# Performance work log

Hardware: AMD Instinct MI355X
Metric: run time of the kernel (lower is better)

## Reference

```python
import jax, jax.numpy as jnp
import numpy as np

T, B, DIN, DLAT = 512, 64, 256, 512

def setup_inputs() -> dict:
    key = jax.random.key(0)
    ks = jax.random.split(key, 5)
    return {
        "x": jax.random.normal(ks[0], (T, B, DIN), dtype=jnp.float32),
        "h0": jax.random.normal(ks[1], (B, DLAT), dtype=jnp.float32),
        "W_in": jax.random.normal(ks[2], (DLAT, DIN), dtype=jnp.float32) * (1.0 / np.sqrt(DIN)),
        "W_h": jax.random.normal(ks[3], (DLAT, DLAT), dtype=jnp.float32) * (1.0 / np.sqrt(DLAT)),
        "b_h": jax.random.normal(ks[4], (DLAT,), dtype=jnp.float32) * 0.01,
    }

def reference(x, h0, W_in, W_h, b_h):
    # x: [T, B, dim_in]; h0: [B, dim_latent]
    # one_step: relu(x @ W_in^T + h @ W_h^T + b_h); stack hidden states over time
    def step(h, x_t):
        h_new = jax.nn.relu(x_t @ W_in.T + h @ W_h.T + b_h)
        return h_new, h_new
    _, h_seq = jax.lax.scan(step, h0, x)  # h_seq: [T, B, dim_latent]
    return h_seq
```

## Files before the change

kernel.cpp:

```cpp
#include <hip/hip_runtime.h>

#define TSTEPS 512
#define BATCH  64
#define DIN    256
#define DLAT   512

typedef _Float16 half8_t __attribute__((ext_vector_type(8)));
typedef float    f32x4  __attribute__((ext_vector_type(4)));

#define WS_WF_OFF  (512u * 1024u)
#define WS_TIER2   (512u * 1024u)
#define WS_TIER1   (768u * 1024u)

__device__ __forceinline__ void barrier_lds_only()
{
    __builtin_amdgcn_sched_barrier(0);
    asm volatile("s_waitcnt lgkmcnt(0)\n\ts_barrier" ::: "memory");
    __builtin_amdgcn_sched_barrier(0);
}

#define BM 64
#define BN 64
#define BK 32

__global__ __launch_bounds__(256)
void precompute_gemm(const float* __restrict__ x,
                     const float* __restrict__ Win,
                     const float* __restrict__ bh,
                     float* __restrict__ P)
{
    __shared__ float As[BM][BK + 1];
    __shared__ float Ws[BN][BK + 1];
    const int m0  = blockIdx.y * BM;
    const int n0  = blockIdx.x * BN;
    const int tid = threadIdx.x;
    const int tx  = tid & 15;
    const int ty  = tid >> 4;
    const int lr  = tid >> 2;
    const int lc  = (tid & 3) * 8;

    float acc[4][4] = {};

    for (int kk = 0; kk < DIN; kk += BK) {
        const float* ax = x   + (size_t)(m0 + lr) * DIN + kk + lc;
        const float* aw = Win + (size_t)(n0 + lr) * DIN + kk + lc;
        float4 a0 = *(const float4*)(ax);
        float4 a1 = *(const float4*)(ax + 4);
        float4 w0 = *(const float4*)(aw);
        float4 w1 = *(const float4*)(aw + 4);
        As[lr][lc+0]=a0.x; As[lr][lc+1]=a0.y; As[lr][lc+2]=a0.z; As[lr][lc+3]=a0.w;
        As[lr][lc+4]=a1.x; As[lr][lc+5]=a1.y; As[lr][lc+6]=a1.z; As[lr][lc+7]=a1.w;
        Ws[lr][lc+0]=w0.x; Ws[lr][lc+1]=w0.y; Ws[lr][lc+2]=w0.z; Ws[lr][lc+3]=w0.w;
        Ws[lr][lc+4]=w1.x; Ws[lr][lc+5]=w1.y; Ws[lr][lc+6]=w1.z; Ws[lr][lc+7]=w1.w;
        __syncthreads();
        #pragma unroll
        for (int k = 0; k < BK; ++k) {
            float a[4], w[4];
            #pragma unroll
            for (int i = 0; i < 4; ++i) a[i] = As[ty*4+i][k];
            #pragma unroll
            for (int j = 0; j < 4; ++j) w[j] = Ws[tx*4+j][k];
            #pragma unroll
            for (int i = 0; i < 4; ++i)
                #pragma unroll
                for (int j = 0; j < 4; ++j)
                    acc[i][j] += a[i] * w[j];
        }
        __syncthreads();
    }

    float4 bv = *(const float4*)(bh + n0 + tx*4);
    #pragma unroll
    for (int i = 0; i < 4; ++i) {
        float4 v;
        v.x = acc[i][0] + bv.x; v.y = acc[i][1] + bv.y;
        v.z = acc[i][2] + bv.z; v.w = acc[i][3] + bv.w;
        *(float4*)(P + (size_t)(m0 + ty*4 + i) * DLAT + n0 + tx*4) = v;
    }
}

__global__ __launch_bounds__(256)
void pack_wh_mfma(const float* __restrict__ Wh, _Float16* __restrict__ Wm)
{
    const int idx  = blockIdx.x * 256 + threadIdx.x;
    const int lane = idx & 63;
    const int tile = idx >> 6;
    const int kt   = tile >> 5;
    const int ntg  = tile & 31;
    const int n    = ntg * 16 + (lane & 15);
    const int k0   = kt * 32 + (lane >> 4) * 8;
    half8_t v;
    #pragma unroll
    for (int e = 0; e < 8; ++e)
        v[e] = (_Float16)Wh[(size_t)n * DLAT + k0 + e];
    *(half8_t*)(Wm + (size_t)idx * 8) = v;
}

__global__ __launch_bounds__(256)
void pack_win_f16(const float* __restrict__ Win, _Float16* __restrict__ Wf)
{
    const int idx  = blockIdx.x * 256 + threadIdx.x;
    const int lane = idx & 63;
    const int tile = idx >> 6;
    const int kt   = tile >> 5;
    const int ntg  = tile & 31;
    const int n    = ntg * 16 + (lane & 15);
    const int k0   = kt * 32 + (lane >> 4) * 8;
    half8_t v;
    #pragma unroll
    for (int e = 0; e < 8; ++e)
        v[e] = (_Float16)Win[(size_t)n * DIN + k0 + e];
    *(half8_t*)(Wf + (size_t)idx * 8) = v;
}

__global__ __launch_bounds__(256)
void precompute_mfma(const float* __restrict__ x,
                     const half8_t* __restrict__ Wf,
                     const float* __restrict__ bh,
                     float* __restrict__ P)
{
    const int tid  = threadIdx.x;
    const int wave = tid >> 6, lane = tid & 63;
    const int wm   = wave >> 1, wn = wave & 1;
    const int m0   = (blockIdx.x >> 2) * 128 + wm * 64;
    const int n0   = (blockIdx.x & 3) * 128 + wn * 64;
    const int col  = lane & 15, rg = lane >> 4;

    float bv[4];
    #pragma unroll
    for (int nt = 0; nt < 4; ++nt) bv[nt] = bh[n0 + nt * 16 + col];

    f32x4 C[4][4] = {};

    #pragma unroll
    for (int kt = 0; kt < 8; ++kt) {
        half8_t A[4];
        #pragma unroll
        for (int mt = 0; mt < 4; ++mt) {
            const float* xp = x + (size_t)(m0 + mt * 16 + col) * DIN
                                + kt * 32 + rg * 8;
            float4 a = *(const float4*)xp;
            float4 b = *(const float4*)(xp + 4);
            half8_t v;
            v[0] = (_Float16)a.x; v[1] = (_Float16)a.y;
            v[2] = (_Float16)a.z; v[3] = (_Float16)a.w;
            v[4] = (_Float16)b.x; v[5] = (_Float16)b.y;
            v[6] = (_Float16)b.z; v[7] = (_Float16)b.w;
            A[mt] = v;
        }
        half8_t B[4];
        #pragma unroll
        for (int nt = 0; nt < 4; ++nt)
            B[nt] = Wf[(size_t)((kt * 32 + (n0 >> 4) + nt) * 64) + lane];
        #pragma unroll
        for (int mt = 0; mt < 4; ++mt)
            #pragma unroll
            for (int nt = 0; nt < 4; ++nt)
                C[mt][nt] = __builtin_amdgcn_mfma_f32_16x16x32_f16(
                                A[mt], B[nt], C[mt][nt], 0, 0, 0);
    }

    #pragma unroll
    for (int mt = 0; mt < 4; ++mt)
        #pragma unroll
        for (int nt = 0; nt < 4; ++nt) {
            #pragma unroll
            for (int r = 0; r < 4; ++r) {
                const int m = m0 + mt * 16 + rg * 4 + r;
                P[(size_t)m * DLAT + n0 + nt * 16 + col] = C[mt][nt][r] + bv[nt];
            }
        }
}

__global__ __launch_bounds__(512, 2)
void rnn_scan_pf(const half8_t* __restrict__ Wm,
                 const float* __restrict__ h0,
                 float* __restrict__ out)
{
    __shared__ half8_t  ldsB[8 * 16 * 64];
    __shared__ _Float16 hbuf[2][DLAT];

    const int b    = blockIdx.x;
    const int tid  = threadIdx.x;
    const int w    = tid >> 6;
    const int lane = tid & 63;
    const int kt0  = 2 * w;
    const int aoff = (lane >> 4) * 8;

    half8_t bfr[48];
    #pragma unroll
    for (int s = 0; s < 16; ++s) {
        const int c  = s >> 1;
        const int kt = (kt0 + s) & 15;
        #pragma unroll
        for (int nt = 0; nt < 4; ++nt) {
            half8_t v = Wm[(size_t)((kt * 32 + w * 4 + nt) * 64) + lane];
            if ((s & 1) && nt >= 2) ldsB[(w * 16 + c * 2 + (nt - 2)) * 64 + lane] = v;
            else                    bfr[c * 6 + ((s & 1) ? 4 + nt : nt)] = v;
        }
    }

    hbuf[0][tid] = (_Float16)h0[(size_t)b * DLAT + tid];
    __syncthreads();

    half8_t Ap[2][2], Bp[2];
    #pragma unroll
    for (int i = 0; i < 4; ++i)
        Ap[i >> 1][i & 1] =
            *(const half8_t*)&hbuf[0][((kt0 + i) & 15) * 32 + aoff];
    Bp[0] = ldsB[(w * 16 + 0) * 64 + lane];
    Bp[1] = ldsB[(w * 16 + 1) * 64 + lane];

    for (int t = 0; t < TSTEPS; ++t) {
        const int cur = t & 1, nxt = cur ^ 1;
        float* orow = out + ((size_t)t * BATCH + b) * DLAT;
        float pv = orow[w * 64 + lane];

        f32x4 C[4] = {};
        __builtin_amdgcn_s_setprio(1);
        #pragma unroll
        for (int c = 0; c < 8; ++c) {
            const int pb = c & 1;
            #pragma unroll
            for (int nt = 0; nt < 4; ++nt)
                C[nt] = __builtin_amdgcn_mfma_f32_16x16x32_f16(
                            Ap[pb][0], bfr[c * 6 + nt], C[nt], 0, 0, 0);
            C[0] = __builtin_amdgcn_mfma_f32_16x16x32_f16(
                        Ap[pb][1], bfr[c * 6 + 4], C[0], 0, 0, 0);
            C[1] = __builtin_amdgcn_mfma_f32_16x16x32_f16(
                        Ap[pb][1], bfr[c * 6 + 5], C[1], 0, 0, 0);
            C[2] = __builtin_amdgcn_mfma_f32_16x16x32_f16(
                        Ap[pb][1], Bp[0], C[2], 0, 0, 0);
            C[3] = __builtin_amdgcn_mfma_f32_16x16x32_f16(
                        Ap[pb][1], Bp[1], C[3], 0, 0, 0);
            if (c < 7) {
                Bp[0] = ldsB[(w * 16 + (c + 1) * 2 + 0) * 64 + lane];
                Bp[1] = ldsB[(w * 16 + (c + 1) * 2 + 1) * 64 + lane];
            }
            if (c < 6) {
                #pragma unroll
                for (int i = 0; i < 2; ++i) {
                    const int s = (c + 2) * 2 + i;
                    Ap[pb][i] =
                        *(const half8_t*)&hbuf[cur][((kt0 + s) & 15) * 32 + aoff];
                }
            }
        }
        __builtin_amdgcn_s_setprio(0);

        const int g4 = lane >> 4;
        float m = (g4 == 0) ? C[0][0]
                : (g4 == 1) ? C[1][0]
                : (g4 == 2) ? C[2][0]
                :             C[3][0];
        float v = fmaxf(m + pv, 0.f);
        orow[w * 64 + lane] = v;
        hbuf[nxt][w * 64 + lane] = (_Float16)v;

        Ap[0][0] = *(const half8_t*)&hbuf[nxt][((kt0 + 0) & 15) * 32 + aoff];
        Ap[0][1] = *(const half8_t*)&hbuf[nxt][((kt0 + 1) & 15) * 32 + aoff];
        Bp[0] = ldsB[(w * 16 + 0) * 64 + lane];
        Bp[1] = ldsB[(w * 16 + 1) * 64 + lane];

        barrier_lds_only();

        Ap[1][0] = *(const half8_t*)&hbuf[nxt][((kt0 + 2) & 15) * 32 + aoff];
        Ap[1][1] = *(const half8_t*)&hbuf[nxt][((kt0 + 3) & 15) * 32 + aoff];
    }
}

__global__ __launch_bounds__(512)
void rnn_scan_row(const float* __restrict__ Wh,
                  const float* __restrict__ h0,
                  float* __restrict__ out)
{
    __shared__ float h[DLAT];
    const int b = blockIdx.x;
    const int r = threadIdx.x;
    h[r] = h0[(size_t)b * DLAT + r];
    __syncthreads();
    const float* wrow = Wh + (size_t)r * DLAT;
    for (int t = 0; t < TSTEPS; ++t) {
        float* orow = out + ((size_t)t * BATCH + b) * DLAT;
        float acc = orow[r];
        #pragma unroll 8
        for (int k = 0; k < DLAT; k += 4) {
            float4 w  = *(const float4*)(wrow + k);
            float4 hv = *(const float4*)&h[k];
            acc += w.x*hv.x + w.y*hv.y + w.z*hv.z + w.w*hv.w;
        }
        float v = fmaxf(acc, 0.f);
        __syncthreads();
        h[r] = v;
        orow[r] = v;
        __syncthreads();
    }
}

extern "C" void kernel_launch(void* const* d_in, const int* in_sizes, int n_in,
                              void* d_out, int out_size, void* d_ws, size_t ws_size,
                              hipStream_t stream)
{
    const float* x    = (const float*)d_in[0];
    const float* h0   = (const float*)d_in[1];
    const float* Win  = (const float*)d_in[2];
    const float* Wh   = (const float*)d_in[3];
    const float* bh   = (const float*)d_in[4];
    float* out = (float*)d_out;

    if (ws_size >= WS_TIER1) {
        _Float16* Wm = (_Float16*)d_ws;
        _Float16* Wf = (_Float16*)((char*)d_ws + WS_WF_OFF);
        pack_wh_mfma<<<128, 256, 0, stream>>>(Wh, Wm);
        pack_win_f16<<<64, 256, 0, stream>>>(Win, Wf);
        precompute_mfma<<<1024, 256, 0, stream>>>(x, (const half8_t*)Wf, bh, out);
        rnn_scan_pf<<<BATCH, 512, 0, stream>>>((const half8_t*)Wm, h0, out);
    } else if (ws_size >= WS_TIER2) {
        _Float16* Wm = (_Float16*)d_ws;
        dim3 gA(DLAT / BN, (TSTEPS * BATCH) / BM);
        pack_wh_mfma<<<128, 256, 0, stream>>>(Wh, Wm);
        precompute_gemm<<<gA, 256, 0, stream>>>(x, Win, bh, out);
        rnn_scan_pf<<<BATCH, 512, 0, stream>>>((const half8_t*)Wm, h0, out);
    } else {
        dim3 gA(DLAT / BN, (TSTEPS * BATCH) / BM);
        precompute_gemm<<<gA, 256, 0, stream>>>(x, Win, bh, out);
        rnn_scan_row<<<BATCH, 512, 0, stream>>>(Wh, h0, out);
    }
}
```

Measured before the change: 676.2 us.

## Run own-wave MFMA chunk before barrier and prefetch next-step input projection

Each wave's first K-chunk reads only the hidden-state slice that the same wave just wrote. The recurrent scan now issues those eight MFMAs before the per-step LDS barrier instead of after it. This takes part of the matrix work off the serial barrier-to-barrier critical path of every timestep. The precomputed input projection for the next timestep is also loaded from global memory one step early, so its latency is hidden behind the current step. The cost is more live registers and a peeled prologue, and correctness depends on the chunk-0 k-tiles staying within the wave's own output slice.

```diff
diff --git a/kernel.cpp b/kernel.cpp
--- a/kernel.cpp
+++ b/kernel.cpp
@@ -173,7 +173,7 @@
 }
 
 __global__ __launch_bounds__(512, 2)
-void rnn_scan_pf(const half8_t* __restrict__ Wm,
+void rnn_scan_pb(const half8_t* __restrict__ Wm,
                  const float* __restrict__ h0,
                  float* __restrict__ out)
 {
@@ -203,23 +203,39 @@
     hbuf[0][tid] = (_Float16)h0[(size_t)b * DLAT + tid];
     __syncthreads();
 
+#define CHUNK0_EXEC()                                                          \
+    do {                                                                       \
+        C[0] = __builtin_amdgcn_mfma_f32_16x16x32_f16(Ap[0][0], bfr[0], C[0], 0, 0, 0); \
+        C[1] = __builtin_amdgcn_mfma_f32_16x16x32_f16(Ap[0][0], bfr[1], C[1], 0, 0, 0); \
+        C[2] = __builtin_amdgcn_mfma_f32_16x16x32_f16(Ap[0][0], bfr[2], C[2], 0, 0, 0); \
+        C[3] = __builtin_amdgcn_mfma_f32_16x16x32_f16(Ap[0][0], bfr[3], C[3], 0, 0, 0); \
+        C[0] = __builtin_amdgcn_mfma_f32_16x16x32_f16(Ap[0][1], bfr[4], C[0], 0, 0, 0); \
+        C[1] = __builtin_amdgcn_mfma_f32_16x16x32_f16(Ap[0][1], bfr[5], C[1], 0, 0, 0); \
+        C[2] = __builtin_amdgcn_mfma_f32_16x16x32_f16(Ap[0][1], Bp[0],  C[2], 0, 0, 0); \
+        C[3] = __builtin_amdgcn_mfma_f32_16x16x32_f16(Ap[0][1], Bp[1],  C[3], 0, 0, 0); \
+    } while (0)
+
     half8_t Ap[2][2], Bp[2];
-    #pragma unroll
-    for (int i = 0; i < 4; ++i)
-        Ap[i >> 1][i & 1] =
-            *(const half8_t*)&hbuf[0][((kt0 + i) & 15) * 32 + aoff];
+    f32x4 C[4] = {};
+    Ap[0][0] = *(const half8_t*)&hbuf[0][((kt0 + 0) & 15) * 32 + aoff];
+    Ap[0][1] = *(const half8_t*)&hbuf[0][((kt0 + 1) & 15) * 32 + aoff];
     Bp[0] = ldsB[(w * 16 + 0) * 64 + lane];
     Bp[1] = ldsB[(w * 16 + 1) * 64 + lane];
+    CHUNK0_EXEC();
+    Bp[0] = ldsB[(w * 16 + 2) * 64 + lane];
+    Bp[1] = ldsB[(w * 16 + 3) * 64 + lane];
+    Ap[1][0] = *(const half8_t*)&hbuf[0][((kt0 + 2) & 15) * 32 + aoff];
+    Ap[1][1] = *(const half8_t*)&hbuf[0][((kt0 + 3) & 15) * 32 + aoff];
+    Ap[0][0] = *(const half8_t*)&hbuf[0][((kt0 + 4) & 15) * 32 + aoff];
+    Ap[0][1] = *(const half8_t*)&hbuf[0][((kt0 + 5) & 15) * 32 + aoff];
+    float pvt = out[(size_t)0 * BATCH * DLAT + (size_t)b * DLAT + w * 64 + lane];
 
     for (int t = 0; t < TSTEPS; ++t) {
         const int cur = t & 1, nxt = cur ^ 1;
-        float* orow = out + ((size_t)t * BATCH + b) * DLAT;
-        float pv = orow[w * 64 + lane];
-
-        f32x4 C[4] = {};
+
         __builtin_amdgcn_s_setprio(1);
         #pragma unroll
-        for (int c = 0; c < 8; ++c) {
+        for (int c = 1; c < 8; ++c) {
             const int pb = c & 1;
             #pragma unroll
             for (int nt = 0; nt < 4; ++nt)
@@ -237,7 +253,7 @@
                 Bp[0] = ldsB[(w * 16 + (c + 1) * 2 + 0) * 64 + lane];
                 Bp[1] = ldsB[(w * 16 + (c + 1) * 2 + 1) * 64 + lane];
             }
-            if (c < 6) {
+            if (c >= 1 && c < 6) {
                 #pragma unroll
                 for (int i = 0; i < 2; ++i) {
                     const int s = (c + 2) * 2 + i;
@@ -253,20 +269,31 @@
                 : (g4 == 1) ? C[1][0]
                 : (g4 == 2) ? C[2][0]
                 :             C[3][0];
-        float v = fmaxf(m + pv, 0.f);
+        float v = fmaxf(m + pvt, 0.f);
+        float* orow = out + ((size_t)t * BATCH + b) * DLAT;
         orow[w * 64 + lane] = v;
         hbuf[nxt][w * 64 + lane] = (_Float16)v;
 
+        const int t2 = (t + 1 < TSTEPS) ? t + 1 : t;
+        pvt = out[((size_t)t2 * BATCH + b) * DLAT + w * 64 + lane];
         Ap[0][0] = *(const half8_t*)&hbuf[nxt][((kt0 + 0) & 15) * 32 + aoff];
         Ap[0][1] = *(const half8_t*)&hbuf[nxt][((kt0 + 1) & 15) * 32 + aoff];
         Bp[0] = ldsB[(w * 16 + 0) * 64 + lane];
         Bp[1] = ldsB[(w * 16 + 1) * 64 + lane];
+        #pragma unroll
+        for (int nt = 0; nt < 4; ++nt) C[nt] = (f32x4){0.f, 0.f, 0.f, 0.f};
+        CHUNK0_EXEC();
+        Bp[0] = ldsB[(w * 16 + 2) * 64 + lane];
+        Bp[1] = ldsB[(w * 16 + 3) * 64 + lane];
 
         barrier_lds_only();
 
         Ap[1][0] = *(const half8_t*)&hbuf[nxt][((kt0 + 2) & 15) * 32 + aoff];
         Ap[1][1] = *(const half8_t*)&hbuf[nxt][((kt0 + 3) & 15) * 32 + aoff];
-    }
+        Ap[0][0] = *(const half8_t*)&hbuf[nxt][((kt0 + 4) & 15) * 32 + aoff];
+        Ap[0][1] = *(const half8_t*)&hbuf[nxt][((kt0 + 5) & 15) * 32 + aoff];
+    }
+#undef CHUNK0_EXEC
 }
 
 __global__ __launch_bounds__(512)
@@ -314,13 +341,13 @@
         pack_wh_mfma<<<128, 256, 0, stream>>>(Wh, Wm);
         pack_win_f16<<<64, 256, 0, stream>>>(Win, Wf);
         precompute_mfma<<<1024, 256, 0, stream>>>(x, (const half8_t*)Wf, bh, out);
-        rnn_scan_pf<<<BATCH, 512, 0, stream>>>((const half8_t*)Wm, h0, out);
+        rnn_scan_pb<<<BATCH, 512, 0, stream>>>((const half8_t*)Wm, h0, out);
     } else if (ws_size >= WS_TIER2) {
         _Float16* Wm = (_Float16*)d_ws;
         dim3 gA(DLAT / BN, (TSTEPS * BATCH) / BM);
         pack_wh_mfma<<<128, 256, 0, stream>>>(Wh, Wm);
         precompute_gemm<<<gA, 256, 0, stream>>>(x, Win, bh, out);
-        rnn_scan_pf<<<BATCH, 512, 0, stream>>>((const half8_t*)Wm, h0, out);
+        rnn_scan_pb<<<BATCH, 512, 0, stream>>>((const half8_t*)Wm, h0, out);
     } else {
         dim3 gA(DLAT / BN, (TSTEPS * BATCH) / BM);
         precompute_gemm<<<gA, 256, 0, stream>>>(x, Win, bh, out);
```

New measurement: 637.6 us. 5.7% less time.
